# Performance work log

Measured on AMD Instinct MI355X. Metric: run time of the kernel, lower is better.

## Reference

```python
import jax, jax.numpy as jnp
import numpy as np

B, S, F, H = 2048, 512, 64, 256

def setup_inputs() -> dict:
    key = jax.random.key(0)
    ks = jax.random.split(key, 9)
    s = 0.05
    return {
        "x": jax.random.normal(ks[0], (B, S, F), jnp.float32),
        "h0": jax.random.normal(ks[1], (1, B, H), jnp.float32),
        "c0": jax.random.normal(ks[2], (1, B, H), jnp.float32),
        "W_ih": jax.random.normal(ks[3], (4 * H, F), jnp.float32) * s,
        "W_hh": jax.random.normal(ks[4], (4 * H, H), jnp.float32) * s,
        "b_ih": jax.random.normal(ks[5], (4 * H,), jnp.float32) * s,
        "b_hh": jax.random.normal(ks[6], (4 * H,), jnp.float32) * s,
        "W_dense": jax.random.normal(ks[7], (F, H), jnp.float32) * s,
        "b_dense": jax.random.normal(ks[8], (F,), jnp.float32) * s,
        "seq_len": S,
    }

def reference(x, h0, c0, W_ih, W_hh, b_ih, b_hh, W_dense, b_dense, seq_len):
    # h_0 tensors are [1, B, H]; original squeezes dim 0.
    h = h0[0]
    c = c0[0]
    bias = b_ih + b_hh  # [4H]
    Hd = W_hh.shape[1]

    def dense(v):  # [B, H] -> [B, F]
        return v @ W_dense.T + b_dense

    # epsilon = 0.0 => teacher forcing never used; next input is dense(c_t).
    x_t = dense(h)

    def step(carry, _):
        h, c, x_t = carry
        gates = x_t @ W_ih.T + h @ W_hh.T + bias  # [B, 4H]
        i = jax.nn.sigmoid(gates[:, 0 * Hd:1 * Hd])
        f = jax.nn.sigmoid(gates[:, 1 * Hd:2 * Hd])
        g = jnp.tanh(gates[:, 2 * Hd:3 * Hd])
        o = jax.nn.sigmoid(gates[:, 3 * Hd:4 * Hd])
        c_new = f * c + i * g
        h_new = o * jnp.tanh(c_new)
        # Original: h_t = (h', c'); x_t = dense(h_t[1]) = dense(c'); output[:, t] = dense(c')
        y = c_new @ W_dense.T + b_dense
        return (h_new, c_new, y), y

    (_, _, _), ys = jax.lax.scan(step, (h, c, x_t), None, length=seq_len)
    # ys: [S, B, F] -> [B, S, F]
    return jnp.transpose(ys, (1, 0, 2))
```

## Files before the change

kernel.cpp:

```cpp
#include <hip/hip_runtime.h>
#include <stdint.h>

#define SEQ   512
#define FD    64
#define HD    256
#define ZSTR  324
#define CSTR  260

#define HC_ELEMS 2560
#define WS_DENSE_ELEM (128 * HC_ELEMS)

typedef __attribute__((ext_vector_type(8))) __bf16 bf16x8;
typedef __attribute__((ext_vector_type(4))) float  f32x4;

__device__ __forceinline__ int hc_slot(int w, int idx) {
    const int R = (w < 4) ? 3 : 5;
    if (idx < R)     return (w < 4 ? w * 3 : 12 + (w - 4) * 5) + idx;
    if (idx < R + 3) return 32 + w * 3 + (idx - R);
    return 56 + (w < 4 ? w * 10 : 40 + (w - 4) * 8) + (idx - R - 3);
}

__device__ __forceinline__ float sigm(float x) {
    return __builtin_amdgcn_rcpf(1.0f + __expf(-x));
}
__device__ __forceinline__ float tanh_(float x) {
    return 2.0f * __builtin_amdgcn_rcpf(1.0f + __expf(-2.0f * x)) - 1.0f;
}

__global__ __launch_bounds__(64) void prep_weights(
    const float* __restrict__ W_ih, const float* __restrict__ W_hh,
    const float* __restrict__ W_dense, __bf16* __restrict__ wsb)
{
    const int b = blockIdx.x, l = threadIdx.x, lr = l & 15, lg = l >> 4;
    if (b < 128) {
        const int w = b >> 4, idx = b & 15;
        const int s = 2 * w + (idx >> 3), nt = (idx >> 1) & 3, h = idx & 1;
        const int n = nt * 256 + s * 16 + lr;
        const int slot = hc_slot(w, idx);
        for (int c = 0; c < 5; ++c) {
            const int k0 = h * 160 + c * 32 + lg * 8;
            const float* src = (k0 < 64) ? (W_ih + n * 64 + k0)
                                         : (W_hh + n * 256 + (k0 - 64));
            bf16x8 v;
            for (int e = 0; e < 8; ++e) v[e] = (__bf16)src[e];
            *(bf16x8*)(wsb + (size_t)slot * HC_ELEMS + c * 512 + l * 8) = v;
        }
    } else {
        const int d = b - 128;
        const int f = d * 16 + lr;
        for (int c = 0; c < 8; ++c) {
            const float* src = W_dense + f * 256 + c * 32 + lg * 8;
            bf16x8 v;
            for (int e = 0; e < 8; ++e) v[e] = (__bf16)src[e];
            *(bf16x8*)(wsb + WS_DENSE_ELEM + d * 4096 + c * 512 + l * 8) = v;
        }
    }
}


template<int R, bool DENSE>
__device__ __forceinline__ void run_loop(
    bf16x8 (&wall)[25], const __bf16* __restrict__ wsb,
    const __bf16* __restrict__ WLDS, __bf16* __restrict__ Zb, __bf16* __restrict__ CBb,
    float (&creg)[2][4], const float (&biasv)[2][4], float ybias,
    float* __restrict__ outp, int w, int lr, int lg, int l)
{
    constexpr int NS = 16 - R - 3;
    const __bf16* wstr_base = wsb +
        (size_t)(56 + (w < 4 ? w * 10 : 40 + (w - 4) * 8)) * HC_ELEMS + l * 8;
    const __bf16* wlds_base = WLDS + (size_t)(w * 3) * HC_ELEMS + l * 8;

    for (int t = 0; t < SEQ; ++t) {
        __syncthreads();

        const __bf16* Zc = Zb + (t & 1) * (16 * ZSTR);
        __bf16*       Zn = Zb + ((t + 1) & 1) * (16 * ZSTR);

        const __bf16* wstr = wstr_base;
        asm volatile("" : "+v"(wstr));

        bf16x8 sb0[5], sb1[5];
#define LOADSTR(BUF, I) { _Pragma("unroll") \
        for (int c = 0; c < 5; ++c) BUF[c] = *(const bf16x8*)(wstr + (I) * HC_ELEMS + c * 512); }
        LOADSTR(sb0, 0)
        LOADSTR(sb1, 1)

        bf16x8 a[10];
#pragma unroll
        for (int ks = 0; ks < 10; ++ks)
            a[ks] = *(const bf16x8*)(&Zc[lr * ZSTR + ks * 32 + lg * 8]);

        f32x4 acc[4];
        int scnt = 0;
#pragma unroll
        for (int idx = 0; idx < 16; ++idx) {
            const int p = idx >> 3, nt = (idx >> 1) & 3, h = idx & 1;
            const float bb = biasv[p][nt];
            f32x4 cc = (h == 0) ? f32x4{bb, bb, bb, bb} : acc[nt];

#define MFMA5(SRC) { _Pragma("unroll") \
            for (int c = 0; c < 5; ++c) \
                cc = __builtin_amdgcn_mfma_f32_16x16x32_bf16(a[h * 5 + c], SRC, cc, 0, 0, 0); }

            if (idx < R) {
                MFMA5(wall[idx * 5 + c])
            } else if (idx < R + 3) {
                bf16x8 ld[5];
#pragma unroll
                for (int c = 0; c < 5; ++c)
                    ld[c] = *(const bf16x8*)(wlds_base + (idx - R) * HC_ELEMS + c * 512);
                MFMA5(ld[c])
            } else {
                if (scnt & 1) {
                    MFMA5(sb1[c])
                    if (scnt + 2 < NS) LOADSTR(sb1, scnt + 2)
                } else {
                    MFMA5(sb0[c])
                    if (scnt + 2 < NS) LOADSTR(sb0, scnt + 2)
                }
                ++scnt;
            }
            acc[nt] = cc;

            if ((idx & 7) == 7) {
                const int jj = (2 * w + p) * 16 + lr;
#pragma unroll
                for (int r = 0; r < 4; ++r) {
                    const int m = lg * 4 + r;
                    const float ig = sigm(acc[0][r]);
                    const float fg = sigm(acc[1][r]);
                    const float gg = tanh_(acc[2][r]);
                    const float og = sigm(acc[3][r]);
                    const float cn = fg * creg[p][r] + ig * gg;
                    creg[p][r] = cn;
                    const float hn = og * tanh_(cn);
                    Zn[m * ZSTR + 64 + jj] = (__bf16)hn;
                    CBb[m * CSTR + jj]     = (__bf16)cn;
                }
            }
        }

        __syncthreads();

        if (DENSE) {
            f32x4 ya = {ybias, ybias, ybias, ybias};
#pragma unroll
            for (int c = 0; c < 8; ++c) {
                bf16x8 acb = *(const bf16x8*)(&CBb[lr * CSTR + c * 32 + lg * 8]);
                ya = __builtin_amdgcn_mfma_f32_16x16x32_bf16(acb, wall[R * 5 + c], ya, 0, 0, 0);
            }
            const int f = w * 16 + lr;
#pragma unroll
            for (int r = 0; r < 4; ++r) {
                const int m = lg * 4 + r;
                outp[(size_t)m * (SEQ * FD) + t * FD + f] = ya[r];
                Zn[m * ZSTR + f] = (__bf16)ya[r];
            }
        }
    }
#undef MFMA5
#undef LOADSTR
}

__global__ __launch_bounds__(512) __attribute__((amdgpu_waves_per_eu(2, 2)))
void lstm_persist(
    const float* __restrict__ h0, const float* __restrict__ c0,
    const float* __restrict__ b_ih, const float* __restrict__ b_hh,
    const float* __restrict__ b_dense, const __bf16* __restrict__ wsb,
    float* __restrict__ out)
{
    __shared__ __align__(16) __bf16 WLDS[24 * HC_ELEMS];
    __shared__ __align__(16) __bf16 Zb[2 * 16 * ZSTR];
    __shared__ __align__(16) __bf16 CBb[16 * CSTR];

    const int tid = threadIdx.x;
    const int w   = tid >> 6;
    const int l   = tid & 63;
    const int lr  = l & 15;
    const int lg  = l >> 4;
    const int row0 = blockIdx.x * 16;
    const int R = (w < 4) ? 3 : 5;

    bf16x8 wall[25];
    if (w < 4) {
#pragma unroll
        for (int i = 0; i < 3; ++i)
#pragma unroll
            for (int c = 0; c < 5; ++c)
                wall[i * 5 + c] = *(const bf16x8*)(wsb + (size_t)hc_slot(w, i) * HC_ELEMS + c * 512 + l * 8);
#pragma unroll
        for (int c = 0; c < 8; ++c)
            wall[15 + c] = *(const bf16x8*)(wsb + WS_DENSE_ELEM + w * 4096 + c * 512 + l * 8);
    } else {
#pragma unroll
        for (int i = 0; i < 5; ++i)
#pragma unroll
            for (int c = 0; c < 5; ++c)
                wall[i * 5 + c] = *(const bf16x8*)(wsb + (size_t)hc_slot(w, i) * HC_ELEMS + c * 512 + l * 8);
    }

#pragma unroll
    for (int i = 0; i < 3; ++i)
#pragma unroll
        for (int c = 0; c < 5; ++c)
            *(bf16x8*)(WLDS + (size_t)(w * 3 + i) * HC_ELEMS + c * 512 + l * 8) =
                *(const bf16x8*)(wsb + (size_t)hc_slot(w, R + i) * HC_ELEMS + c * 512 + l * 8);

    float biasv[2][4];
    float creg[2][4];
#pragma unroll
    for (int p = 0; p < 2; ++p) {
        const int jj = (2 * w + p) * 16 + lr;
#pragma unroll
        for (int nt = 0; nt < 4; ++nt) {
            const int n = nt * 256 + jj;
            biasv[p][nt] = b_ih[n] + b_hh[n];
        }
#pragma unroll
        for (int r = 0; r < 4; ++r)
            creg[p][r] = c0[(size_t)(row0 + lg * 4 + r) * HD + jj];
    }
    float ybias = (w < 4) ? b_dense[w * 16 + lr] : 0.0f;

    {
        const int e0 = tid * 8;
        const int m  = e0 >> 8;
        const int jj = e0 & 255;
        const float4 h1 = *(const float4*)(h0 + (size_t)(row0 + m) * HD + jj);
        const float4 h2 = *(const float4*)(h0 + (size_t)(row0 + m) * HD + jj + 4);
        __bf16* zp = &Zb[m * ZSTR + 64 + jj];
        zp[0] = (__bf16)h1.x; zp[1] = (__bf16)h1.y; zp[2] = (__bf16)h1.z; zp[3] = (__bf16)h1.w;
        zp[4] = (__bf16)h2.x; zp[5] = (__bf16)h2.y; zp[6] = (__bf16)h2.z; zp[7] = (__bf16)h2.w;
    }
    __syncthreads();

    if (w < 4) {
        f32x4 ya = {ybias, ybias, ybias, ybias};
#pragma unroll
        for (int c = 0; c < 8; ++c) {
            bf16x8 av = *(const bf16x8*)(&Zb[lr * ZSTR + 64 + c * 32 + lg * 8]);
            ya = __builtin_amdgcn_mfma_f32_16x16x32_bf16(av, wall[15 + c], ya, 0, 0, 0);
        }
#pragma unroll
        for (int r = 0; r < 4; ++r)
            Zb[(lg * 4 + r) * ZSTR + w * 16 + lr] = (__bf16)ya[r];
    }

    float* outp = out + (size_t)row0 * SEQ * FD;

    if (w < 4) run_loop<3, true >(wall, wsb, WLDS, Zb, CBb, creg, biasv, ybias, outp, w, lr, lg, l);
    else       run_loop<5, false>(wall, wsb, WLDS, Zb, CBb, creg, biasv, ybias, outp, w, lr, lg, l);
}

extern "C" void kernel_launch(void* const* d_in, const int* in_sizes, int n_in,
                              void* d_out, int out_size, void* d_ws, size_t ws_size,
                              hipStream_t stream) {
    (void)in_sizes; (void)n_in; (void)ws_size; (void)out_size;
    const float* h0      = (const float*)d_in[1];
    const float* c0      = (const float*)d_in[2];
    const float* W_ih    = (const float*)d_in[3];
    const float* W_hh    = (const float*)d_in[4];
    const float* b_ih    = (const float*)d_in[5];
    const float* b_hh    = (const float*)d_in[6];
    const float* W_dense = (const float*)d_in[7];
    const float* b_dense = (const float*)d_in[8];
    __bf16* wsb = (__bf16*)d_ws;

    prep_weights<<<132, 64, 0, stream>>>(W_ih, W_hh, W_dense, wsb);
    lstm_persist<<<128, 512, 0, stream>>>(h0, c0, b_ih, b_hh, b_dense, wsb, (float*)d_out);
}
```

Baseline: 3.358 ms.

## Stream all gate weights via global_load_lds ring buffer instead of register/LDS residency

Replaces the mixed scheme (weights pinned in registers, partly in static LDS, partly streamed from global into registers) with a uniform per-wave triple-buffered LDS ring. The ring is filled every timestep by direct global-to-LDS DMA loads, with explicit vmcnt waits. This frees the large register array and simplifies the weight layout, and dense weights are now reloaded from global each step. The cost is re-fetching all weights from L2 every timestep, which could make the kernel bandwidth- or latency-bound.

```diff
diff --git a/kernel.cpp b/kernel.cpp
--- a/kernel.cpp
+++ b/kernel.cpp
@@ -7,24 +7,25 @@
 #define ZSTR  324
 #define CSTR  260
 
-#define HC_ELEMS 2560
-#define WS_DENSE_ELEM (128 * HC_ELEMS)
+#define GRPB      5120
+#define WGB       (16 * GRPB)
+#define DENSE_OFF (8 * WGB)
+#define RING_D    3
 
 typedef __attribute__((ext_vector_type(8))) __bf16 bf16x8;
 typedef __attribute__((ext_vector_type(4))) float  f32x4;
 
-__device__ __forceinline__ int hc_slot(int w, int idx) {
-    const int R = (w < 4) ? 3 : 5;
-    if (idx < R)     return (w < 4 ? w * 3 : 12 + (w - 4) * 5) + idx;
-    if (idx < R + 3) return 32 + w * 3 + (idx - R);
-    return 56 + (w < 4 ? w * 10 : 40 + (w - 4) * 8) + (idx - R - 3);
-}
-
 __device__ __forceinline__ float sigm(float x) {
     return __builtin_amdgcn_rcpf(1.0f + __expf(-x));
 }
 __device__ __forceinline__ float tanh_(float x) {
     return 2.0f * __builtin_amdgcn_rcpf(1.0f + __expf(-2.0f * x)) - 1.0f;
+}
+
+__device__ __forceinline__ void dma16(const void* g, void* l) {
+    __builtin_amdgcn_global_load_lds(
+        (const __attribute__((address_space(1))) int*)g,
+        (__attribute__((address_space(3))) int*)l, 16, 0, 0);
 }
 
 __global__ __launch_bounds__(64) void prep_weights(
@@ -33,17 +34,16 @@
 {
     const int b = blockIdx.x, l = threadIdx.x, lr = l & 15, lg = l >> 4;
     if (b < 128) {
-        const int w = b >> 4, idx = b & 15;
-        const int s = 2 * w + (idx >> 3), nt = (idx >> 1) & 3, h = idx & 1;
+        const int w = b >> 4, i = b & 15;
+        const int s = 2 * w + (i >> 3), h = (i >> 2) & 1, nt = i & 3;
         const int n = nt * 256 + s * 16 + lr;
-        const int slot = hc_slot(w, idx);
         for (int c = 0; c < 5; ++c) {
             const int k0 = h * 160 + c * 32 + lg * 8;
             const float* src = (k0 < 64) ? (W_ih + n * 64 + k0)
                                          : (W_hh + n * 256 + (k0 - 64));
             bf16x8 v;
             for (int e = 0; e < 8; ++e) v[e] = (__bf16)src[e];
-            *(bf16x8*)(wsb + (size_t)slot * HC_ELEMS + c * 512 + l * 8) = v;
+            *(bf16x8*)(wsb + (size_t)((w * 16 + i) * 5 + c) * 512 + l * 8) = v;
         }
     } else {
         const int d = b - 128;
@@ -52,23 +52,75 @@
             const float* src = W_dense + f * 256 + c * 32 + lg * 8;
             bf16x8 v;
             for (int e = 0; e < 8; ++e) v[e] = (__bf16)src[e];
-            *(bf16x8*)(wsb + WS_DENSE_ELEM + d * 4096 + c * 512 + l * 8) = v;
-        }
-    }
-}
-
-
-template<int R, bool DENSE>
-__device__ __forceinline__ void run_loop(
-    bf16x8 (&wall)[25], const __bf16* __restrict__ wsb,
-    const __bf16* __restrict__ WLDS, __bf16* __restrict__ Zb, __bf16* __restrict__ CBb,
-    float (&creg)[2][4], const float (&biasv)[2][4], float ybias,
-    float* __restrict__ outp, int w, int lr, int lg, int l)
+            *(bf16x8*)(wsb + DENSE_OFF / 2 + d * 4096 + c * 512 + l * 8) = v;
+        }
+    }
+}
+
+__global__ __launch_bounds__(512) __attribute__((amdgpu_waves_per_eu(2, 2)))
+void lstm_persist(
+    const float* __restrict__ h0, const float* __restrict__ c0,
+    const float* __restrict__ b_ih, const float* __restrict__ b_hh,
+    const float* __restrict__ b_dense, const __bf16* __restrict__ wsb,
+    float* __restrict__ out)
 {
-    constexpr int NS = 16 - R - 3;
-    const __bf16* wstr_base = wsb +
-        (size_t)(56 + (w < 4 ? w * 10 : 40 + (w - 4) * 8)) * HC_ELEMS + l * 8;
-    const __bf16* wlds_base = WLDS + (size_t)(w * 3) * HC_ELEMS + l * 8;
+    __shared__ __align__(1024) char  RING[8 * RING_D * GRPB];
+    __shared__ __align__(16) __bf16 Zb[2 * 16 * ZSTR];
+    __shared__ __align__(16) __bf16 CBb[16 * CSTR];
+
+    const int tid = threadIdx.x;
+    const int w   = tid >> 6;
+    const int l   = tid & 63;
+    const int lr  = l & 15;
+    const int lg  = l >> 4;
+    const int row0 = blockIdx.x * 16;
+
+    const char*   wgbase = (const char*)wsb + (size_t)w * WGB;
+    char*         ringw  = RING + w * (RING_D * GRPB);
+    const __bf16* wdbase = wsb + DENSE_OFF / 2 + w * 4096 + l * 8;
+
+    float biasv[2][4];
+    float creg[2][4];
+#pragma unroll
+    for (int p = 0; p < 2; ++p) {
+        const int jj = (2 * w + p) * 16 + lr;
+#pragma unroll
+        for (int nt = 0; nt < 4; ++nt) {
+            const int n = nt * 256 + jj;
+            biasv[p][nt] = b_ih[n] + b_hh[n];
+        }
+#pragma unroll
+        for (int r = 0; r < 4; ++r)
+            creg[p][r] = c0[(size_t)(row0 + lg * 4 + r) * HD + jj];
+    }
+    float ybias = (w < 4) ? b_dense[w * 16 + lr] : 0.0f;
+
+    {
+        const int e0 = tid * 8;
+        const int m  = e0 >> 8;
+        const int jj = e0 & 255;
+        const float4 h1 = *(const float4*)(h0 + (size_t)(row0 + m) * HD + jj);
+        const float4 h2 = *(const float4*)(h0 + (size_t)(row0 + m) * HD + jj + 4);
+        __bf16* zp = &Zb[m * ZSTR + 64 + jj];
+        zp[0] = (__bf16)h1.x; zp[1] = (__bf16)h1.y; zp[2] = (__bf16)h1.z; zp[3] = (__bf16)h1.w;
+        zp[4] = (__bf16)h2.x; zp[5] = (__bf16)h2.y; zp[6] = (__bf16)h2.z; zp[7] = (__bf16)h2.w;
+    }
+    __syncthreads();
+
+    if (w < 4) {
+        f32x4 ya = {ybias, ybias, ybias, ybias};
+#pragma unroll
+        for (int c = 0; c < 8; ++c) {
+            bf16x8 wdc = *(const bf16x8*)(wdbase + c * 512);
+            bf16x8 av  = *(const bf16x8*)(&Zb[lr * ZSTR + 64 + c * 32 + lg * 8]);
+            ya = __builtin_amdgcn_mfma_f32_16x16x32_bf16(av, wdc, ya, 0, 0, 0);
+        }
+#pragma unroll
+        for (int r = 0; r < 4; ++r)
+            Zb[(lg * 4 + r) * ZSTR + w * 16 + lr] = (__bf16)ya[r];
+    }
+
+    float* outp = out + (size_t)row0 * SEQ * FD;
 
     for (int t = 0; t < SEQ; ++t) {
         __syncthreads();
@@ -76,53 +128,58 @@
         const __bf16* Zc = Zb + (t & 1) * (16 * ZSTR);
         __bf16*       Zn = Zb + ((t + 1) & 1) * (16 * ZSTR);
 
-        const __bf16* wstr = wstr_base;
-        asm volatile("" : "+v"(wstr));
-
-        bf16x8 sb0[5], sb1[5];
-#define LOADSTR(BUF, I) { _Pragma("unroll") \
-        for (int c = 0; c < 5; ++c) BUF[c] = *(const bf16x8*)(wstr + (I) * HC_ELEMS + c * 512); }
-        LOADSTR(sb0, 0)
-        LOADSTR(sb1, 1)
-
-        bf16x8 a[10];
-#pragma unroll
-        for (int ks = 0; ks < 10; ++ks)
-            a[ks] = *(const bf16x8*)(&Zc[lr * ZSTR + ks * 32 + lg * 8]);
-
-        f32x4 acc[4];
-        int scnt = 0;
-#pragma unroll
-        for (int idx = 0; idx < 16; ++idx) {
-            const int p = idx >> 3, nt = (idx >> 1) & 3, h = idx & 1;
+        const char* gp = wgbase + (size_t)l * 16;
+        asm volatile("" : "+v"(gp));
+
+#pragma unroll
+        for (int c = 0; c < 10; ++c) {
+            dma16(gp, ringw + (c / 5) * GRPB + (c % 5) * 1024);
+            gp += 1024;
+        }
+
+        bf16x8 aph[5];
+        f32x4  acc[4];
+
+#pragma unroll
+        for (int i = 0; i < 16; ++i) {
+            const int p = i >> 3, h = (i >> 2) & 1, nt = i & 3;
+
+            if ((i & 3) == 0) {
+#pragma unroll
+                for (int c = 0; c < 5; ++c)
+                    aph[c] = *(const bf16x8*)(&Zc[lr * ZSTR + (h * 5 + c) * 32 + lg * 8]);
+            }
+
+            if (i + 2 < 16) {
+#pragma unroll
+                for (int c = 0; c < 5; ++c) {
+                    dma16(gp, ringw + ((i + 2) % 3) * GRPB + c * 1024);
+                    gp += 1024;
+                }
+            }
+
+            if (i <= 13)      asm volatile("s_waitcnt vmcnt(10)" ::: "memory");
+            else if (i == 14) asm volatile("s_waitcnt vmcnt(5)"  ::: "memory");
+            else              asm volatile("s_waitcnt vmcnt(0)"  ::: "memory");
+            __builtin_amdgcn_sched_barrier(0);
+
+            const char* slot = ringw + (i % 3) * GRPB;
+            bf16x8 b0 = *(const bf16x8*)(slot + 0 * 1024 + l * 16);
+            bf16x8 b1 = *(const bf16x8*)(slot + 1 * 1024 + l * 16);
+            bf16x8 b2 = *(const bf16x8*)(slot + 2 * 1024 + l * 16);
+            bf16x8 b3 = *(const bf16x8*)(slot + 3 * 1024 + l * 16);
+            bf16x8 b4 = *(const bf16x8*)(slot + 4 * 1024 + l * 16);
+
             const float bb = biasv[p][nt];
             f32x4 cc = (h == 0) ? f32x4{bb, bb, bb, bb} : acc[nt];
-
-#define MFMA5(SRC) { _Pragma("unroll") \
-            for (int c = 0; c < 5; ++c) \
-                cc = __builtin_amdgcn_mfma_f32_16x16x32_bf16(a[h * 5 + c], SRC, cc, 0, 0, 0); }
-
-            if (idx < R) {
-                MFMA5(wall[idx * 5 + c])
-            } else if (idx < R + 3) {
-                bf16x8 ld[5];
-#pragma unroll
-                for (int c = 0; c < 5; ++c)
-                    ld[c] = *(const bf16x8*)(wlds_base + (idx - R) * HC_ELEMS + c * 512);
-                MFMA5(ld[c])
-            } else {
-                if (scnt & 1) {
-                    MFMA5(sb1[c])
-                    if (scnt + 2 < NS) LOADSTR(sb1, scnt + 2)
-                } else {
-                    MFMA5(sb0[c])
-                    if (scnt + 2 < NS) LOADSTR(sb0, scnt + 2)
-                }
-                ++scnt;
-            }
+            cc = __builtin_amdgcn_mfma_f32_16x16x32_bf16(aph[0], b0, cc, 0, 0, 0);
+            cc = __builtin_amdgcn_mfma_f32_16x16x32_bf16(aph[1], b1, cc, 0, 0, 0);
+            cc = __builtin_amdgcn_mfma_f32_16x16x32_bf16(aph[2], b2, cc, 0, 0, 0);
+            cc = __builtin_amdgcn_mfma_f32_16x16x32_bf16(aph[3], b3, cc, 0, 0, 0);
+            cc = __builtin_amdgcn_mfma_f32_16x16x32_bf16(aph[4], b4, cc, 0, 0, 0);
             acc[nt] = cc;
 
-            if ((idx & 7) == 7) {
+            if ((i & 7) == 7) {
                 const int jj = (2 * w + p) * 16 + lr;
 #pragma unroll
                 for (int r = 0; r < 4; ++r) {
@@ -142,12 +199,15 @@
 
         __syncthreads();
 
-        if (DENSE) {
+        if (w < 4) {
+            const __bf16* wdp = wdbase;
+            asm volatile("" : "+v"(wdp));
             f32x4 ya = {ybias, ybias, ybias, ybias};
 #pragma unroll
             for (int c = 0; c < 8; ++c) {
+                bf16x8 wdc = *(const bf16x8*)(wdp + c * 512);
                 bf16x8 acb = *(const bf16x8*)(&CBb[lr * CSTR + c * 32 + lg * 8]);
-                ya = __builtin_amdgcn_mfma_f32_16x16x32_bf16(acb, wall[R * 5 + c], ya, 0, 0, 0);
+                ya = __builtin_amdgcn_mfma_f32_16x16x32_bf16(acb, wdc, ya, 0, 0, 0);
             }
             const int f = w * 16 + lr;
 #pragma unroll
@@ -158,98 +218,6 @@
             }
         }
     }
-#undef MFMA5
-#undef LOADSTR
-}
-
-__global__ __launch_bounds__(512) __attribute__((amdgpu_waves_per_eu(2, 2)))
-void lstm_persist(
-    const float* __restrict__ h0, const float* __restrict__ c0,
-    const float* __restrict__ b_ih, const float* __restrict__ b_hh,
-    const float* __restrict__ b_dense, const __bf16* __restrict__ wsb,
-    float* __restrict__ out)
-{
-    __shared__ __align__(16) __bf16 WLDS[24 * HC_ELEMS];
-    __shared__ __align__(16) __bf16 Zb[2 * 16 * ZSTR];
-    __shared__ __align__(16) __bf16 CBb[16 * CSTR];
-
-    const int tid = threadIdx.x;
-    const int w   = tid >> 6;
-    const int l   = tid & 63;
-    const int lr  = l & 15;
-    const int lg  = l >> 4;
-    const int row0 = blockIdx.x * 16;
-    const int R = (w < 4) ? 3 : 5;
-
-    bf16x8 wall[25];
-    if (w < 4) {
-#pragma unroll
-        for (int i = 0; i < 3; ++i)
-#pragma unroll
-            for (int c = 0; c < 5; ++c)
-                wall[i * 5 + c] = *(const bf16x8*)(wsb + (size_t)hc_slot(w, i) * HC_ELEMS + c * 512 + l * 8);
-#pragma unroll
-        for (int c = 0; c < 8; ++c)
-            wall[15 + c] = *(const bf16x8*)(wsb + WS_DENSE_ELEM + w * 4096 + c * 512 + l * 8);
-    } else {
-#pragma unroll
-        for (int i = 0; i < 5; ++i)
-#pragma unroll
-            for (int c = 0; c < 5; ++c)
-                wall[i * 5 + c] = *(const bf16x8*)(wsb + (size_t)hc_slot(w, i) * HC_ELEMS + c * 512 + l * 8);
-    }
-
-#pragma unroll
-    for (int i = 0; i < 3; ++i)
-#pragma unroll
-        for (int c = 0; c < 5; ++c)
-            *(bf16x8*)(WLDS + (size_t)(w * 3 + i) * HC_ELEMS + c * 512 + l * 8) =
-                *(const bf16x8*)(wsb + (size_t)hc_slot(w, R + i) * HC_ELEMS + c * 512 + l * 8);
-
-    float biasv[2][4];
-    float creg[2][4];
-#pragma unroll
-    for (int p = 0; p < 2; ++p) {
-        const int jj = (2 * w + p) * 16 + lr;
-#pragma unroll
-        for (int nt = 0; nt < 4; ++nt) {
-            const int n = nt * 256 + jj;
-            biasv[p][nt] = b_ih[n] + b_hh[n];
-        }
-#pragma unroll
-        for (int r = 0; r < 4; ++r)
-            creg[p][r] = c0[(size_t)(row0 + lg * 4 + r) * HD + jj];
-    }
-    float ybias = (w < 4) ? b_dense[w * 16 + lr] : 0.0f;
-
-    {
-        const int e0 = tid * 8;
-        const int m  = e0 >> 8;
-        const int jj = e0 & 255;
-        const float4 h1 = *(const float4*)(h0 + (size_t)(row0 + m) * HD + jj);
-        const float4 h2 = *(const float4*)(h0 + (size_t)(row0 + m) * HD + jj + 4);
-        __bf16* zp = &Zb[m * ZSTR + 64 + jj];
-        zp[0] = (__bf16)h1.x; zp[1] = (__bf16)h1.y; zp[2] = (__bf16)h1.z; zp[3] = (__bf16)h1.w;
-        zp[4] = (__bf16)h2.x; zp[5] = (__bf16)h2.y; zp[6] = (__bf16)h2.z; zp[7] = (__bf16)h2.w;
-    }
-    __syncthreads();
-
-    if (w < 4) {
-        f32x4 ya = {ybias, ybias, ybias, ybias};
-#pragma unroll
-        for (int c = 0; c < 8; ++c) {
-            bf16x8 av = *(const bf16x8*)(&Zb[lr * ZSTR + 64 + c * 32 + lg * 8]);
-            ya = __builtin_amdgcn_mfma_f32_16x16x32_bf16(av, wall[15 + c], ya, 0, 0, 0);
-        }
-#pragma unroll
-        for (int r = 0; r < 4; ++r)
-            Zb[(lg * 4 + r) * ZSTR + w * 16 + lr] = (__bf16)ya[r];
-    }
-
-    float* outp = out + (size_t)row0 * SEQ * FD;
-
-    if (w < 4) run_loop<3, true >(wall, wsb, WLDS, Zb, CBb, creg, biasv, ybias, outp, w, lr, lg, l);
-    else       run_loop<5, false>(wall, wsb, WLDS, Zb, CBb, creg, biasv, ybias, outp, w, lr, lg, l);
 }
 
 extern "C" void kernel_launch(void* const* d_in, const int* in_sizes, int n_in,
```

Result: slower. 4.487 ms (+33.6%).
